# Kernel optimization log

Hardware: AMD Instinct MI355X
Metric: run time of the kernel (lower is better)

## Reference

```python
import jax, jax.numpy as jnp
import numpy as np
import math

D_MODEL = 2048
NUM_HEADS = 16
D_HEAD = D_MODEL // NUM_HEADS
MAX_SEQ_LEN = 2048
THETA = 10000.0
B, T = 2, 2048


def setup_inputs() -> dict:
    key = jax.random.key(0)
    ks = jax.random.split(key, 5)
    s = 1.0 / math.sqrt(D_MODEL)
    return {
        "x": jax.random.normal(ks[0], (B, T, D_MODEL), dtype=jnp.float32),
        "token_positions": jnp.arange(T, dtype=jnp.int64 if jax.config.jax_enable_x64 else jnp.int32),
        "Wq": jax.random.normal(ks[1], (D_MODEL, D_MODEL), dtype=jnp.float32) * s,
        "Wk": jax.random.normal(ks[2], (D_MODEL, D_MODEL), dtype=jnp.float32) * s,
        "Wv": jax.random.normal(ks[3], (D_MODEL, D_MODEL), dtype=jnp.float32) * s,
        "Wproj": jax.random.normal(ks[4], (D_MODEL, D_MODEL), dtype=jnp.float32) * s,
    }


def _rope_tables(dtype):
    inv_freq = 1.0 / (THETA ** (jnp.arange(0, D_HEAD, 2, dtype=jnp.float32) / D_HEAD))
    angle = jnp.arange(MAX_SEQ_LEN, dtype=jnp.float32)[:, None] * inv_freq[None, :]  # [S, d/2]
    return jnp.cos(angle).astype(dtype), jnp.sin(angle).astype(dtype)


def _apply_rope(x, cos, sin):
    # x: [B, H, T, d_head]; cos/sin: [T, d_head/2] (broadcast over B,H)
    x1 = x[..., 0::2]
    x2 = x[..., 1::2]
    o1 = x1 * cos - x2 * sin
    o2 = x1 * sin + x2 * cos
    return jnp.stack([o1, o2], axis=-1).reshape(x.shape)


def reference(x, token_positions, Wq, Wk, Wv, Wproj):
    Bx, Tx, D = x.shape
    # Linear layers: weight [out, in], no bias
    q = (x @ Wq.T).reshape(Bx, Tx, NUM_HEADS, D_HEAD).transpose(0, 2, 1, 3)
    k = (x @ Wk.T).reshape(Bx, Tx, NUM_HEADS, D_HEAD).transpose(0, 2, 1, 3)
    v = (x @ Wv.T).reshape(Bx, Tx, NUM_HEADS, D_HEAD).transpose(0, 2, 1, 3)

    cos_t, sin_t = _rope_tables(x.dtype)
    cos = cos_t[token_positions]  # [T, d_head/2]
    sin = sin_t[token_positions]
    q = _apply_rope(q, cos, sin)
    k = _apply_rope(k, cos, sin)

    scale = 1.0 / math.sqrt(D_HEAD)
    scores = jnp.einsum("bhqd,bhkd->bhqk", q, k) * scale
    causal = jnp.tril(jnp.ones((Tx, Tx), dtype=bool))
    scores = jnp.where(causal, scores, -jnp.inf)
    attn = jax.nn.softmax(scores, axis=-1)
    o = jnp.einsum("bhqk,bhkd->bhqd", attn, v)  # [B, H, T, d_head]
    o = o.transpose(0, 2, 1, 3).reshape(Bx, Tx, D)
    return o @ Wproj.T
```

## Files before the change

kernel.cpp:

```cpp
#include <hip/hip_runtime.h>
#include <hip/hip_bf16.h>

#define DM    2048
#define NH    16
#define DHD   128
#define TSEQ  2048
#define NBB   2
#define NTOK  (NBB*TSEQ)

typedef __attribute__((ext_vector_type(8))) short bf16x8;
typedef __attribute__((ext_vector_type(4))) float f32x4;

typedef __attribute__((address_space(1))) const void GVoid;
typedef __attribute__((address_space(3))) void LVoid;
#define GLOAD16(SRC, DST) __builtin_amdgcn_global_load_lds((GVoid*)(SRC), (LVoid*)(DST), 16, 0, 0)

__device__ __forceinline__ unsigned short f2bf(float f) {
  union { float f; unsigned u; } v; v.f = f;
  unsigned r = v.u + 0x7fffu + ((v.u >> 16) & 1u);
  return (unsigned short)(r >> 16);
}
__device__ __forceinline__ float bf2f(unsigned short h) {
  union { unsigned u; float f; } v; v.u = ((unsigned)h) << 16;
  return v.f;
}

#define QSCALE (0.08838834764831845f * 1.4426950408889634f)

__global__ void cvt_kernel(const float* __restrict__ in, unsigned short* __restrict__ out, int n4) {
  int i = blockIdx.x * blockDim.x + threadIdx.x;
  int stride = gridDim.x * blockDim.x;
  for (; i < n4; i += stride) {
    float4 v = reinterpret_cast<const float4*>(in)[i];
    ushort4 o;
    o.x = f2bf(v.x); o.y = f2bf(v.y); o.z = f2bf(v.z); o.w = f2bf(v.w);
    reinterpret_cast<ushort4*>(out)[i] = o;
  }
}

__global__ void cvt4_kernel(const float* __restrict__ a, const float* __restrict__ b,
                           const float* __restrict__ c, const float* __restrict__ d,
                           unsigned short* __restrict__ out, int n4per) {
  const float* in = (blockIdx.y == 0) ? a : (blockIdx.y == 1) ? b : (blockIdx.y == 2) ? c : d;
  unsigned short* o = out + (size_t)blockIdx.y * (size_t)n4per * 4;
  int i = blockIdx.x * blockDim.x + threadIdx.x;
  int stride = gridDim.x * blockDim.x;
  for (; i < n4per; i += stride) {
    float4 v = reinterpret_cast<const float4*>(in)[i];
    ushort4 ov;
    ov.x = f2bf(v.x); ov.y = f2bf(v.y); ov.z = f2bf(v.z); ov.w = f2bf(v.w);
    reinterpret_cast<ushort4*>(o)[i] = ov;
  }
}

__global__ void rope_table_kernel(const int* __restrict__ pos, float* __restrict__ ctab, float* __restrict__ stab) {
  int idx = blockIdx.x * blockDim.x + threadIdx.x;
  if (idx >= TSEQ * 64) return;
  int i = idx & 63;
  int t = idx >> 6;
  float freq = expf(-(2.0f * i / 128.0f) * 9.210340371976184f);
  float ang = (float)pos[t] * freq;
  ctab[idx] = cosf(ang);
  stab[idx] = sinf(ang);
}

__global__ void vtrans_kernel(const unsigned short* __restrict__ Vb, unsigned short* __restrict__ VTt) {
  __shared__ unsigned short tile[32][33];
  int t0 = blockIdx.x * 32, d0 = blockIdx.y * 32, bh = blockIdx.z;
  int h = bh & (NH - 1), b = bh >> 4;
  int tx = threadIdx.x, ty = threadIdx.y;
  #pragma unroll
  for (int i = 0; i < 4; i++) {
    int tt = t0 + ty + i * 8;
    tile[ty + i * 8][tx] = Vb[(size_t)(b * TSEQ + tt) * DM + h * DHD + d0 + tx];
  }
  __syncthreads();
  #pragma unroll
  for (int i = 0; i < 4; i++) {
    int d = d0 + ty + i * 8;
    VTt[((size_t)bh * DHD + d) * TSEQ + t0 + tx] = tile[tx][ty + i * 8];
  }
}

#define GBM 256
#define GBN 128
#define GBK 64
template<int MODE>
__global__ __launch_bounds__(512, 2) void gemm256(
    const unsigned short* __restrict__ A,
    const unsigned short* __restrict__ Bt,
    void* __restrict__ Cp,
    unsigned short* __restrict__ QrO, unsigned short* __restrict__ KrO,
    const float* __restrict__ ct, const float* __restrict__ st,
    int K, int N, int NBN) {
  __shared__ unsigned short lds[3 * (GBM + GBN) * GBK];
  const int t = threadIdx.x;
  const int lane = t & 63, w = t >> 6;
  const int wr = w >> 2, wc = w & 3;
  const int lr = lane & 15, lg = lane >> 4;
  const int nwg = gridDim.x;
  const int swz = (blockIdx.x & 7) * (nwg >> 3) + (blockIdx.x >> 3);
  const int m0 = (swz / NBN) * GBM;
  const int n0g = (swz % NBN) * GBN;
  const int NT = K / GBK;

  f32x4 acc[8][2] = {};

  auto stageA = [&](int kt, int b) {
    unsigned short* dst = &lds[b * (GBM + GBN) * GBK];
    const size_t k0 = (size_t)kt * GBK;
    #pragma unroll
    for (int c = 0; c < 4; c++) {
      int i = c * 512 + t;
      int row = i >> 3, slot = i & 7;
      int sslot = slot ^ (row & 7);
      GLOAD16(A + (size_t)(m0 + row) * K + k0 + sslot * 8,
              dst + (size_t)(c * 512 + w * 64) * 8);
    }
  };
  auto stageB = [&](int kt, int b) {
    unsigned short* dst = &lds[b * (GBM + GBN) * GBK + GBM * GBK];
    const size_t k0 = (size_t)kt * GBK;
    #pragma unroll
    for (int c = 0; c < 2; c++) {
      int i = c * 512 + t;
      int row = i >> 3, slot = i & 7;
      int sslot = slot ^ (row & 7);
      GLOAD16(Bt + (size_t)(n0g + row) * K + k0 + sslot * 8,
              dst + (size_t)(c * 512 + w * 64) * 8);
    }
  };

  const unsigned short* bufA = nullptr;
  const unsigned short* bufB = nullptr;
  auto ldA = [&](int mi, int ks) -> bf16x8 {
    int r = wr * 128 + mi * 16 + lr;
    int cb = (ks * 64 + lg * 16) ^ ((r & 7) << 4);
    return *(const bf16x8*)((const char*)bufA + r * 128 + cb);
  };
  auto ldB = [&](int ni, int ks) -> bf16x8 {
    int r = wc * 32 + ni * 16 + lr;
    int cb = (ks * 64 + lg * 16) ^ ((r & 7) << 4);
    return *(const bf16x8*)((const char*)bufB + r * 128 + cb);
  };

  stageA(0, 0); stageB(0, 0);
  stageA(1, 1); stageB(1, 1);

  for (int kt = 0; kt < NT; kt++) {
    if (kt + 1 < NT) { asm volatile("s_waitcnt vmcnt(6)" ::: "memory"); }
    else             { asm volatile("s_waitcnt vmcnt(0)" ::: "memory"); }
    __builtin_amdgcn_s_barrier();
    const int b = kt % 3;
    bufA = &lds[b * (GBM + GBN) * GBK];
    bufB = bufA + GBM * GBK;
    const int kt2 = kt + 2, b2 = kt2 % 3;

    bf16x8 bfr[2][2], afr[4][2];
    #pragma unroll
    for (int ni = 0; ni < 2; ni++)
      #pragma unroll
      for (int ks = 0; ks < 2; ks++) bfr[ni][ks] = ldB(ni, ks);
    #pragma unroll
    for (int mi = 0; mi < 4; mi++)
      #pragma unroll
      for (int ks = 0; ks < 2; ks++) afr[mi][ks] = ldA(mi, ks);
    if (kt2 < NT) stageA(kt2, b2);
    asm volatile("s_waitcnt lgkmcnt(0)" ::: "memory");
    __builtin_amdgcn_sched_barrier(0);
    __builtin_amdgcn_s_setprio(1);
    #pragma unroll
    for (int mi = 0; mi < 4; mi++)
      #pragma unroll
      for (int ni = 0; ni < 2; ni++)
        #pragma unroll
        for (int ks = 0; ks < 2; ks++)
          acc[mi][ni] = __builtin_amdgcn_mfma_f32_16x16x32_bf16(afr[mi][ks], bfr[ni][ks], acc[mi][ni], 0, 0, 0);
    __builtin_amdgcn_s_setprio(0);
    __builtin_amdgcn_s_barrier();

    bf16x8 afr2[4][2];
    #pragma unroll
    for (int mi = 0; mi < 4; mi++)
      #pragma unroll
      for (int ks = 0; ks < 2; ks++) afr2[mi][ks] = ldA(mi + 4, ks);
    if (kt2 < NT) stageB(kt2, b2);
    asm volatile("s_waitcnt lgkmcnt(0)" ::: "memory");
    __builtin_amdgcn_sched_barrier(0);
    __builtin_amdgcn_s_setprio(1);
    #pragma unroll
    for (int mi = 0; mi < 4; mi++)
      #pragma unroll
      for (int ni = 0; ni < 2; ni++)
        #pragma unroll
        for (int ks = 0; ks < 2; ks++)
          acc[mi + 4][ni] = __builtin_amdgcn_mfma_f32_16x16x32_bf16(afr2[mi][ks], bfr[ni][ks], acc[mi + 4][ni], 0, 0, 0);
    __builtin_amdgcn_s_setprio(0);
  }

  if (MODE == 0) {
    #pragma unroll
    for (int mi = 0; mi < 8; mi++)
      #pragma unroll
      for (int j = 0; j < 4; j++) {
        int row = m0 + wr * 128 + mi * 16 + lg * 4 + j;
        #pragma unroll
        for (int ni = 0; ni < 2; ni++) {
          int cg = n0g + wc * 32 + ni * 16 + lr;
          ((float*)Cp)[(size_t)row * N + cg] = acc[mi][ni][j];
        }
      }
  } else {
    const int sel = n0g >> 11;
    if (sel == 2) {
      #pragma unroll
      for (int mi = 0; mi < 8; mi++)
        #pragma unroll
        for (int j = 0; j < 4; j++) {
          int row = m0 + wr * 128 + mi * 16 + lg * 4 + j;
          #pragma unroll
          for (int ni = 0; ni < 2; ni++) {
            int c2 = (n0g + wc * 32 + ni * 16 + lr) & 2047;
            ((unsigned short*)Cp)[(size_t)row * DM + c2] = f2bf(acc[mi][ni][j]);
          }
        }
    } else {
      unsigned short* dst = sel ? KrO : QrO;
      const float qm = sel ? 1.0f : QSCALE;
      #pragma unroll
      for (int mi = 0; mi < 8; mi++)
        #pragma unroll
        for (int j = 0; j < 4; j++) {
          int row = m0 + wr * 128 + mi * 16 + lg * 4 + j;
          int bb = row >> 11, tt = row & (TSEQ - 1);
          #pragma unroll
          for (int ni = 0; ni < 2; ni++) {
            int c2 = (n0g + wc * 32 + ni * 16 + lr) & 2047;
            int d = c2 & 127, hh = c2 >> 7;
            float v = acc[mi][ni][j];
            float px = __shfl_xor(v, 1);
            float cc = ct[tt * 64 + (d >> 1)], ss = st[tt * 64 + (d >> 1)];
            float o = (d & 1) ? (px * ss + v * cc) : (v * cc - px * ss);
            dst[(((size_t)(bb * NH + hh)) * TSEQ + tt) * DHD + d] = f2bf(o * qm);
          }
        }
    }
  }
}

__global__ __launch_bounds__(512, 4) void attn_kernel(
    const unsigned short* __restrict__ Qr,
    const unsigned short* __restrict__ Kr,
    const unsigned short* __restrict__ VTt,
    unsigned short* __restrict__ Oa) {
  __shared__ unsigned short Ks[64 * 128];
  __shared__ unsigned short Vs[128 * 64];
  __shared__ unsigned short Ps[8 * 16 * 64];
  const int t = threadIdx.x;
  const int lane = t & 63, w = t >> 6;
  const int wv = w & 3, half = w >> 2;
  const int lr = lane & 15, lg = lane >> 4;
  const int p = blockIdx.x, bh = blockIdx.y;
  const int qA = p, qB = 31 - p;
  const int myq = half ? qA : qB;
  const int q0 = myq * 64;
  const int nt = myq + 1;
  const int ntB = qB + 1;
  const unsigned short* Qh = Qr + (size_t)bh * TSEQ * DHD;
  const unsigned short* Kh = Kr + (size_t)bh * TSEQ * DHD;
  const unsigned short* Vh = VTt + (size_t)bh * DHD * TSEQ;

  bf16x8 qf[4];
  #pragma unroll
  for (int ks = 0; ks < 4; ks++)
    qf[ks] = *(const bf16x8*)&Qh[((size_t)(q0 + wv * 16 + lr)) * DHD + ks * 32 + lg * 8];

  f32x4 oacc[8] = {};
  float ps[4] = {};
  unsigned short* Pw = &Ps[w * 16 * 64];

  for (int jt = 0; jt < ntB; jt++) {
    const int j0 = jt * 64;
    #pragma unroll
    for (int c = 0; c < 2; c++) {
      int ci = c * 512 + t;
      int row = ci >> 4, slot = ci & 15;
      GLOAD16(Kh + (size_t)(j0 + row) * DHD + (slot ^ (row & 7)) * 8,
              &Ks[(c * 512 + w * 64) * 8]);
    }
    #pragma unroll
    for (int c = 0; c < 2; c++) {
      int ci = c * 512 + t;
      int row = ci >> 3, slot = ci & 7;
      GLOAD16(Vh + (size_t)row * TSEQ + j0 + (slot ^ (row & 7)) * 8,
              &Vs[(c * 512 + w * 64) * 8]);
    }
    __syncthreads();
    if (jt < nt) {
      const bool diag = (jt == nt - 1);
      f32x4 sv[4] = {};
      #pragma unroll
      for (int n = 0; n < 4; n++) {
        #pragma unroll
        for (int ks = 0; ks < 4; ks++) {
          int row = n * 16 + lr;
          int byteoff = row * 256 + (((ks * 64 + lg * 16)) ^ ((row & 7) << 4));
          bf16x8 kf = *(const bf16x8*)((const char*)Ks + byteoff);
          sv[n] = __builtin_amdgcn_mfma_f32_16x16x32_bf16(qf[ks], kf, sv[n], 0, 0, 0);
        }
      }
      if (diag) {
        #pragma unroll
        for (int n = 0; n < 4; n++) {
          int kcol = j0 + n * 16 + lr;
          #pragma unroll
          for (int j = 0; j < 4; j++)
            if (kcol > q0 + wv * 16 + lg * 4 + j) sv[n][j] = -INFINITY;
        }
      }
      #pragma unroll
      for (int n = 0; n < 4; n++) {
        #pragma unroll
        for (int j = 0; j < 4; j++) {
          float pv = exp2f(sv[n][j]);
          ps[j] += pv;
          int prow = lg * 4 + j;
          int pcol = n * 16 + lr;
          int byteoff = (prow * 128 + pcol * 2) ^ ((prow & 7) << 4);
          *(unsigned short*)((char*)Pw + byteoff) = f2bf(pv);
        }
      }
      bf16x8 pa[2];
      #pragma unroll
      for (int kk = 0; kk < 2; kk++) {
        int byteoff = lr * 128 + (((kk * 64 + lg * 16)) ^ ((lr & 7) << 4));
        pa[kk] = *(const bf16x8*)((const char*)Pw + byteoff);
      }
      #pragma unroll
      for (int n2 = 0; n2 < 8; n2++) {
        #pragma unroll
        for (int kk = 0; kk < 2; kk++) {
          int row = n2 * 16 + lr;
          int byteoff = row * 128 + (((kk * 64 + lg * 16)) ^ ((row & 7) << 4));
          bf16x8 vf = *(const bf16x8*)((const char*)Vs + byteoff);
          oacc[n2] = __builtin_amdgcn_mfma_f32_16x16x32_bf16(pa[kk], vf, oacc[n2], 0, 0, 0);
        }
      }
    }
    __syncthreads();
  }

  #pragma unroll
  for (int m = 1; m < 16; m <<= 1)
    #pragma unroll
    for (int j = 0; j < 4; j++) ps[j] += __shfl_xor(ps[j], m);
  const int h = bh & (NH - 1), b = bh >> 4;
  #pragma unroll
  for (int j = 0; j < 4; j++) {
    float inv = 1.0f / ps[j];
    int tt = q0 + wv * 16 + lg * 4 + j;
    size_t base = ((size_t)(b * TSEQ + tt)) * DM + h * DHD;
    #pragma unroll
    for (int n2 = 0; n2 < 8; n2++)
      Oa[base + n2 * 16 + lr] = f2bf(oacc[n2][j] * inv);
  }
}

extern "C" void kernel_launch(void* const* d_in, const int* in_sizes, int n_in,
                              void* d_out, int out_size, void* d_ws, size_t ws_size,
                              hipStream_t stream) {
  const float* x  = (const float*)d_in[0];
  const int*   pos = (const int*)d_in[1];
  const float* Wq = (const float*)d_in[2];
  const float* Wk = (const float*)d_in[3];
  const float* Wv = (const float*)d_in[4];
  const float* Wp = (const float*)d_in[5];
  float* out = (float*)d_out;

  char* wsp = (char*)d_ws;
  auto alloc = [&](size_t bytes) { char* p = wsp; wsp += (bytes + 255) & ~(size_t)255; return p; };
  unsigned short* xb  = (unsigned short*)alloc((size_t)NTOK * DM * 2);
  unsigned short* wqb = (unsigned short*)alloc((size_t)DM * DM * 2);
  unsigned short* wkb = (unsigned short*)alloc((size_t)DM * DM * 2);
  unsigned short* wvb = (unsigned short*)alloc((size_t)DM * DM * 2);
  unsigned short* wpb = (unsigned short*)alloc((size_t)DM * DM * 2);
  unsigned short* Qb  = (unsigned short*)alloc((size_t)NTOK * DM * 2);
  unsigned short* Kb  = (unsigned short*)alloc((size_t)NTOK * DM * 2);
  unsigned short* Vb  = (unsigned short*)alloc((size_t)NTOK * DM * 2);
  unsigned short* VTt = (unsigned short*)alloc((size_t)NTOK * DM * 2);
  float* ctab = (float*)alloc((size_t)TSEQ * 64 * 4);
  float* stab = (float*)alloc((size_t)TSEQ * 64 * 4);
  unsigned short* Oa = xb;
  (void)wkb; (void)wvb;

  int n4x = NTOK * DM / 4, n4w = DM * DM / 4;
  cvt_kernel<<<2048, 256, 0, stream>>>(x, xb, n4x);
  cvt4_kernel<<<dim3(256, 4), 256, 0, stream>>>(Wq, Wk, Wv, Wp, wqb, n4w);
  rope_table_kernel<<<(TSEQ * 64) / 256, 256, 0, stream>>>(pos, ctab, stab);

  gemm256<1><<<(NTOK / GBM) * (3 * DM / GBN), 512, 0, stream>>>(
      xb, wqb, Vb, Qb, Kb, ctab, stab, DM, DM, 3 * DM / GBN);

  vtrans_kernel<<<dim3(TSEQ / 32, DHD / 32, NBB * NH), dim3(32, 8), 0, stream>>>(Vb, VTt);

  attn_kernel<<<dim3(16, NBB * NH), 512, 0, stream>>>(Qb, Kb, VTt, Oa);

  gemm256<0><<<(NTOK / GBM) * (DM / GBN), 512, 0, stream>>>(
      Oa, wpb, out, nullptr, nullptr, nullptr, nullptr, DM, DM, DM / GBN);
}
```

Before: 250.7 us.

## Retile GEMMs to 128x256x32 with single-phase K loop and higher occupancy

The GEMM tile goes from 256x128 with K-step 64 and two half-steps per iteration to 128x256 with K-step 32 and one MFMA phase per iteration. The LDS swizzle and staging are rewritten for the narrower K slice, the accumulator becomes 4x4 per wave, and launch bounds are raised to 4 blocks per CU. The intent is smaller LDS per block and more resident waves to hide latency. In exchange there are twice as many K iterations and barriers, and each LDS fetch feeds less MFMA work.

```diff
diff --git a/kernel.cpp b/kernel.cpp
--- a/kernel.cpp
+++ b/kernel.cpp
@@ -82,18 +82,19 @@
   }
 }
 
-#define GBM 256
-#define GBN 128
-#define GBK 64
+#define GBM 128
+#define GBN 256
+#define GBK 32
+#define LDSB ((GBM + GBN) * GBK)
 template<int MODE>
-__global__ __launch_bounds__(512, 2) void gemm256(
+__global__ __launch_bounds__(512, 4) void gemmk(
     const unsigned short* __restrict__ A,
     const unsigned short* __restrict__ Bt,
     void* __restrict__ Cp,
     unsigned short* __restrict__ QrO, unsigned short* __restrict__ KrO,
     const float* __restrict__ ct, const float* __restrict__ st,
     int K, int N, int NBN) {
-  __shared__ unsigned short lds[3 * (GBM + GBN) * GBK];
+  __shared__ unsigned short lds[3 * LDSB];
   const int t = threadIdx.x;
   const int lane = t & 63, w = t >> 6;
   const int wr = w >> 2, wc = w & 3;
@@ -104,109 +105,73 @@
   const int n0g = (swz % NBN) * GBN;
   const int NT = K / GBK;
 
-  f32x4 acc[8][2] = {};
-
-  auto stageA = [&](int kt, int b) {
-    unsigned short* dst = &lds[b * (GBM + GBN) * GBK];
+  f32x4 acc[4][4] = {};
+
+  auto stage = [&](int kt, int b) {
+    unsigned short* dst = &lds[b * LDSB];
     const size_t k0 = (size_t)kt * GBK;
-    #pragma unroll
-    for (int c = 0; c < 4; c++) {
-      int i = c * 512 + t;
-      int row = i >> 3, slot = i & 7;
-      int sslot = slot ^ (row & 7);
-      GLOAD16(A + (size_t)(m0 + row) * K + k0 + sslot * 8,
-              dst + (size_t)(c * 512 + w * 64) * 8);
+    {
+      int row = t >> 2, slot = t & 3;
+      int ss = slot ^ ((row >> 1) & 3);
+      GLOAD16(A + (size_t)(m0 + row) * K + k0 + ss * 8, dst + (size_t)(w * 64) * 8);
+    }
+    unsigned short* dstB = dst + GBM * GBK;
+    #pragma unroll
+    for (int c = 0; c < 2; c++) {
+      int ci = c * 512 + t;
+      int row = ci >> 2, slot = ci & 3;
+      int ss = slot ^ ((row >> 1) & 3);
+      GLOAD16(Bt + (size_t)(n0g + row) * K + k0 + ss * 8, dstB + (size_t)(c * 512 + w * 64) * 8);
     }
   };
-  auto stageB = [&](int kt, int b) {
-    unsigned short* dst = &lds[b * (GBM + GBN) * GBK + GBM * GBK];
-    const size_t k0 = (size_t)kt * GBK;
-    #pragma unroll
-    for (int c = 0; c < 2; c++) {
-      int i = c * 512 + t;
-      int row = i >> 3, slot = i & 7;
-      int sslot = slot ^ (row & 7);
-      GLOAD16(Bt + (size_t)(n0g + row) * K + k0 + sslot * 8,
-              dst + (size_t)(c * 512 + w * 64) * 8);
-    }
+
+  const unsigned short* buf = nullptr;
+  auto ldA = [&](int mi) -> bf16x8 {
+    int r = wr * 64 + mi * 16 + lr;
+    int cb = (lg * 16) ^ (((r >> 1) & 3) << 4);
+    return *(const bf16x8*)((const char*)buf + r * 64 + cb);
   };
-
-  const unsigned short* bufA = nullptr;
-  const unsigned short* bufB = nullptr;
-  auto ldA = [&](int mi, int ks) -> bf16x8 {
-    int r = wr * 128 + mi * 16 + lr;
-    int cb = (ks * 64 + lg * 16) ^ ((r & 7) << 4);
-    return *(const bf16x8*)((const char*)bufA + r * 128 + cb);
+  auto ldB = [&](int ni) -> bf16x8 {
+    int r = wc * 64 + ni * 16 + lr;
+    int cb = (lg * 16) ^ (((r >> 1) & 3) << 4);
+    return *(const bf16x8*)((const char*)(buf + GBM * GBK) + r * 64 + cb);
   };
-  auto ldB = [&](int ni, int ks) -> bf16x8 {
-    int r = wc * 32 + ni * 16 + lr;
-    int cb = (ks * 64 + lg * 16) ^ ((r & 7) << 4);
-    return *(const bf16x8*)((const char*)bufB + r * 128 + cb);
-  };
-
-  stageA(0, 0); stageB(0, 0);
-  stageA(1, 1); stageB(1, 1);
+
+  stage(0, 0);
+  stage(1, 1);
 
   for (int kt = 0; kt < NT; kt++) {
-    if (kt + 1 < NT) { asm volatile("s_waitcnt vmcnt(6)" ::: "memory"); }
+    if (kt + 1 < NT) { asm volatile("s_waitcnt vmcnt(3)" ::: "memory"); }
     else             { asm volatile("s_waitcnt vmcnt(0)" ::: "memory"); }
     __builtin_amdgcn_s_barrier();
-    const int b = kt % 3;
-    bufA = &lds[b * (GBM + GBN) * GBK];
-    bufB = bufA + GBM * GBK;
-    const int kt2 = kt + 2, b2 = kt2 % 3;
-
-    bf16x8 bfr[2][2], afr[4][2];
-    #pragma unroll
-    for (int ni = 0; ni < 2; ni++)
-      #pragma unroll
-      for (int ks = 0; ks < 2; ks++) bfr[ni][ks] = ldB(ni, ks);
-    #pragma unroll
-    for (int mi = 0; mi < 4; mi++)
-      #pragma unroll
-      for (int ks = 0; ks < 2; ks++) afr[mi][ks] = ldA(mi, ks);
-    if (kt2 < NT) stageA(kt2, b2);
+    buf = &lds[(kt % 3) * LDSB];
+
+    bf16x8 bfr[4], afr[4];
+    #pragma unroll
+    for (int ni = 0; ni < 4; ni++) bfr[ni] = ldB(ni);
+    #pragma unroll
+    for (int mi = 0; mi < 4; mi++) afr[mi] = ldA(mi);
+    if (kt + 2 < NT) stage(kt + 2, (kt + 2) % 3);
     asm volatile("s_waitcnt lgkmcnt(0)" ::: "memory");
     __builtin_amdgcn_sched_barrier(0);
     __builtin_amdgcn_s_setprio(1);
     #pragma unroll
     for (int mi = 0; mi < 4; mi++)
       #pragma unroll
-      for (int ni = 0; ni < 2; ni++)
-        #pragma unroll
-        for (int ks = 0; ks < 2; ks++)
-          acc[mi][ni] = __builtin_amdgcn_mfma_f32_16x16x32_bf16(afr[mi][ks], bfr[ni][ks], acc[mi][ni], 0, 0, 0);
+      for (int ni = 0; ni < 4; ni++)
+        acc[mi][ni] = __builtin_amdgcn_mfma_f32_16x16x32_bf16(afr[mi], bfr[ni], acc[mi][ni], 0, 0, 0);
     __builtin_amdgcn_s_setprio(0);
-    __builtin_amdgcn_s_barrier();
-
-    bf16x8 afr2[4][2];
+  }
+
+  if (MODE == 0) {
     #pragma unroll
     for (int mi = 0; mi < 4; mi++)
       #pragma unroll
-      for (int ks = 0; ks < 2; ks++) afr2[mi][ks] = ldA(mi + 4, ks);
-    if (kt2 < NT) stageB(kt2, b2);
-    asm volatile("s_waitcnt lgkmcnt(0)" ::: "memory");
-    __builtin_amdgcn_sched_barrier(0);
-    __builtin_amdgcn_s_setprio(1);
-    #pragma unroll
-    for (int mi = 0; mi < 4; mi++)
-      #pragma unroll
-      for (int ni = 0; ni < 2; ni++)
-        #pragma unroll
-        for (int ks = 0; ks < 2; ks++)
-          acc[mi + 4][ni] = __builtin_amdgcn_mfma_f32_16x16x32_bf16(afr2[mi][ks], bfr[ni][ks], acc[mi + 4][ni], 0, 0, 0);
-    __builtin_amdgcn_s_setprio(0);
-  }
-
-  if (MODE == 0) {
-    #pragma unroll
-    for (int mi = 0; mi < 8; mi++)
-      #pragma unroll
       for (int j = 0; j < 4; j++) {
-        int row = m0 + wr * 128 + mi * 16 + lg * 4 + j;
-        #pragma unroll
-        for (int ni = 0; ni < 2; ni++) {
-          int cg = n0g + wc * 32 + ni * 16 + lr;
+        int row = m0 + wr * 64 + mi * 16 + lg * 4 + j;
+        #pragma unroll
+        for (int ni = 0; ni < 4; ni++) {
+          int cg = n0g + wc * 64 + ni * 16 + lr;
           ((float*)Cp)[(size_t)row * N + cg] = acc[mi][ni][j];
         }
       }
@@ -214,13 +179,13 @@
     const int sel = n0g >> 11;
     if (sel == 2) {
       #pragma unroll
-      for (int mi = 0; mi < 8; mi++)
+      for (int mi = 0; mi < 4; mi++)
         #pragma unroll
         for (int j = 0; j < 4; j++) {
-          int row = m0 + wr * 128 + mi * 16 + lg * 4 + j;
+          int row = m0 + wr * 64 + mi * 16 + lg * 4 + j;
           #pragma unroll
-          for (int ni = 0; ni < 2; ni++) {
-            int c2 = (n0g + wc * 32 + ni * 16 + lr) & 2047;
+          for (int ni = 0; ni < 4; ni++) {
+            int c2 = (n0g + wc * 64 + ni * 16 + lr) & 2047;
             ((unsigned short*)Cp)[(size_t)row * DM + c2] = f2bf(acc[mi][ni][j]);
           }
         }
@@ -228,14 +193,14 @@
       unsigned short* dst = sel ? KrO : QrO;
       const float qm = sel ? 1.0f : QSCALE;
       #pragma unroll
-      for (int mi = 0; mi < 8; mi++)
+      for (int mi = 0; mi < 4; mi++)
         #pragma unroll
         for (int j = 0; j < 4; j++) {
-          int row = m0 + wr * 128 + mi * 16 + lg * 4 + j;
+          int row = m0 + wr * 64 + mi * 16 + lg * 4 + j;
           int bb = row >> 11, tt = row & (TSEQ - 1);
           #pragma unroll
-          for (int ni = 0; ni < 2; ni++) {
-            int c2 = (n0g + wc * 32 + ni * 16 + lr) & 2047;
+          for (int ni = 0; ni < 4; ni++) {
+            int c2 = (n0g + wc * 64 + ni * 16 + lr) & 2047;
             int d = c2 & 127, hh = c2 >> 7;
             float v = acc[mi][ni][j];
             float px = __shfl_xor(v, 1);
@@ -398,13 +363,13 @@
   cvt4_kernel<<<dim3(256, 4), 256, 0, stream>>>(Wq, Wk, Wv, Wp, wqb, n4w);
   rope_table_kernel<<<(TSEQ * 64) / 256, 256, 0, stream>>>(pos, ctab, stab);
 
-  gemm256<1><<<(NTOK / GBM) * (3 * DM / GBN), 512, 0, stream>>>(
+  gemmk<1><<<(NTOK / GBM) * (3 * DM / GBN), 512, 0, stream>>>(
       xb, wqb, Vb, Qb, Kb, ctab, stab, DM, DM, 3 * DM / GBN);
 
   vtrans_kernel<<<dim3(TSEQ / 32, DHD / 32, NBB * NH), dim3(32, 8), 0, stream>>>(Vb, VTt);
 
   attn_kernel<<<dim3(16, NBB * NH), 512, 0, stream>>>(Qb, Kb, VTt, Oa);
 
-  gemm256<0><<<(NTOK / GBM) * (DM / GBN), 512, 0, stream>>>(
+  gemmk<0><<<(NTOK / GBM) * (DM / GBN), 512, 0, stream>>>(
       Oa, wpb, out, nullptr, nullptr, nullptr, nullptr, DM, DM, DM / GBN);
 }
```

After: 260.3 us. 3.8% more time.
